# Performance work log

Hardware: AMD Instinct MI355X
Metric: run time of the kernel (lower is better)

The kernel has to match this reference:

```python
import jax, jax.numpy as jnp
import numpy as np

TOPK = 32

def topk_signed(x, k):
    # keep k entries with largest |value|, zero the rest (exactly k, scatter semantics)
    _, idx = jax.lax.top_k(jnp.abs(x), k)                       # [B, k]
    B = x.shape[0]
    mask = jnp.zeros(x.shape, dtype=bool).at[jnp.arange(B)[:, None], idx].set(True)
    return x * mask

def setup_inputs() -> dict:
    key = jax.random.key(0)
    k1, k2, k3 = jax.random.split(key, 3)
    B, D, L = 16384, 768, 16384
    x = jax.random.normal(k1, (B, D), dtype=jnp.float32)
    W_enc = jax.random.normal(k2, (L, D), dtype=jnp.float32) / np.sqrt(D)
    W_dec = jax.random.normal(k3, (D, L), dtype=jnp.float32) / np.sqrt(L)
    return {"x": x, "W_enc": W_enc, "W_dec": W_dec}

def reference(x, W_enc, W_dec):
    h = x @ W_enc.T                 # [B, L] encode (no bias)
    a = topk_signed(h, TOPK)        # [B, L] sparse latents
    recon = a @ W_dec.T             # [B, D] decode (no bias)
    return recon, a
```

## Files before the change

kernel.cpp:

```cpp
#include <hip/hip_runtime.h>


#define NB 16384
#define ND 768
#define NL 16384
#define SLOTS 24
#define NSL (64 * SLOTS)
#define ROWS 4
#define EPT 6
#define DLT 0.024f
#define CINB 0x40000000u
#define BNDB 0x20000000u
#define IMSK 0xffffu

typedef unsigned short u16;
typedef short bf16x8_t __attribute__((ext_vector_type(8)));
typedef float f32x4_t __attribute__((ext_vector_type(4)));
typedef unsigned short u16x4_t __attribute__((ext_vector_type(4)));

__device__ __forceinline__ u16 f2bf(float f) {
  union { float f; unsigned u; } x; x.f = f;
  unsigned r = x.u + 0x7fffu + ((x.u >> 16) & 1u);
  return (u16)(r >> 16);
}
__device__ __forceinline__ float bf2f(u16 u) {
  union { unsigned u; float f; } x; x.u = ((unsigned)u) << 16;
  return x.f;
}

__device__ __forceinline__ void async16(u16* lds, const u16* g) {
  __builtin_amdgcn_global_load_lds(
      (const __attribute__((address_space(1))) unsigned int*)g,
      (__attribute__((address_space(3))) unsigned int*)lds, 16, 0, 0);
}

__global__ __launch_bounds__(256) void cvt2_bf16(const float* __restrict__ s0,
                                                 u16* __restrict__ d0,
                                                 const float* __restrict__ s1,
                                                 u16* __restrict__ d1, int n4) {
  int i = blockIdx.x * 256 + threadIdx.x;
  const float* s; u16* d;
  if (i < n4) { s = s0; d = d0; } else { s = s1; d = d1; i -= n4; }
  const float4 v = ((const float4*)s)[i];
  u16x4_t o;
  o.x = f2bf(v.x); o.y = f2bf(v.y); o.z = f2bf(v.z); o.w = f2bf(v.w);
  ((u16x4_t*)d)[i] = o;
}

__global__ __launch_bounds__(512, 2) void enc_gemm(const u16* __restrict__ A,
                                                   const u16* __restrict__ Bm,
                                                   unsigned* __restrict__ Lst) {
  __shared__ u16 Ax[2][2][8192];
  __shared__ u16 Bx[2][2][8192];
  __shared__ unsigned rcnt[256];
  __shared__ unsigned slots[256 * SLOTS];

  const int tid  = threadIdx.x;
  const int lane = tid & 63;
  const int w    = tid >> 6;
  const int wr   = w >> 2;
  const int wc   = w & 3;

  const int linear = blockIdx.y * gridDim.x + blockIdx.x;
  const int xcd = linear & 7;
  const int j   = linear >> 3;
  const int hh  = j >> 8;
  const int jj  = j & 255;
  const int cg  = jj >> 5;
  const int rr_ = jj & 3;
  const int cc_ = (jj >> 2) & 7;
  const int brow = (xcd * 8 + hh * 4 + rr_) * 256;
  const int bcol = (cg * 8 + cc_) * 256;

  if (tid < 256) rcnt[tid] = 0;
#pragma unroll
  for (int i = 0; i < (256 * SLOTS) / 512; ++i) slots[tid + 512 * i] = 0;

  f32x4_t acc[8][4];
#pragma unroll
  for (int m = 0; m < 8; ++m)
#pragma unroll
    for (int n = 0; n < 4; ++n) acc[m][n] = (f32x4_t){0.f, 0.f, 0.f, 0.f};

  const int swz = ((lane & 7) ^ (lane >> 3)) * 8;
  const u16* gA = A  + (size_t)(brow + w * 16 + (lane >> 3)) * ND + swz;
  const u16* gB = Bm + (size_t)(bcol + w * 16 + (lane >> 3)) * ND + swz;

#define STGA(BUF, H, J, KT) \
  async16(&Ax[BUF][H][w * 1024 + (J) * 512], gA + ((H) * 128 + (J) * 8) * ND + (KT) * 64)
#define STGB(BUF, H, J, KT) \
  async16(&Bx[BUF][H][w * 1024 + (J) * 512], gB + ((H) * 128 + (J) * 8) * ND + (KT) * 64)
#define STG8(BUF, KT) { STGA(BUF,0,0,KT); STGA(BUF,0,1,KT); STGA(BUF,1,0,KT); STGA(BUF,1,1,KT); \
                        STGB(BUF,0,0,KT); STGB(BUF,0,1,KT); STGB(BUF,1,0,KT); STGB(BUF,1,1,KT); }

  const int fr  = lane & 15;
  const int q4  = lane >> 4;
  const int frl = fr & 7;
  const int c0  = ((q4)     ^ frl) * 8;
  const int c1  = ((4 + q4) ^ frl) * 8;
  const int bhalf = wc >> 1;
  const int brow0 = (wc & 1) * 64;

  STG8(0, 0);

  bf16x8_t afr[4][2];
  bf16x8_t bfr[2][2][2];

#define MFMA16(QR, QC)                                                        \
  __builtin_amdgcn_s_setprio(1);                                              \
  _Pragma("unroll")                                                           \
  for (int m2 = 0; m2 < 4; ++m2)                                              \
    _Pragma("unroll")                                                         \
    for (int n2 = 0; n2 < 2; ++n2) {                                          \
      acc[(QR)*4+m2][(QC)*2+n2] = __builtin_amdgcn_mfma_f32_16x16x32_bf16(    \
          afr[m2][0], bfr[QC][n2][0], acc[(QR)*4+m2][(QC)*2+n2], 0, 0, 0);    \
      acc[(QR)*4+m2][(QC)*2+n2] = __builtin_amdgcn_mfma_f32_16x16x32_bf16(    \
          afr[m2][1], bfr[QC][n2][1], acc[(QR)*4+m2][(QC)*2+n2], 0, 0, 0);    \
    }                                                                         \
  __builtin_amdgcn_s_setprio(0);

#define LDA(BUF, QR)                                                          \
  _Pragma("unroll")                                                           \
  for (int m2 = 0; m2 < 4; ++m2) {                                            \
    afr[m2][0] = *(const bf16x8_t*)&Ax[BUF][wr][((QR)*64 + m2*16 + fr)*64 + c0]; \
    afr[m2][1] = *(const bf16x8_t*)&Ax[BUF][wr][((QR)*64 + m2*16 + fr)*64 + c1]; \
  }
#define LDB(BUF, QC)                                                          \
  _Pragma("unroll")                                                           \
  for (int n2 = 0; n2 < 2; ++n2) {                                            \
    bfr[QC][n2][0] = *(const bf16x8_t*)&Bx[BUF][bhalf][(brow0 + (QC)*32 + n2*16 + fr)*64 + c0]; \
    bfr[QC][n2][1] = *(const bf16x8_t*)&Bx[BUF][bhalf][(brow0 + (QC)*32 + n2*16 + fr)*64 + c1]; \
  }

#define HALF(BUF)                                                              \
  __builtin_amdgcn_s_barrier();                   \
  __builtin_amdgcn_sched_barrier(0);                                           \
  LDA(BUF, 0); LDB(BUF, 0); MFMA16(0, 0);                                      \
  LDB(BUF, 1); MFMA16(0, 1);                                                   \
  LDA(BUF, 1); MFMA16(1, 0); MFMA16(1, 1);                                     \
  __builtin_amdgcn_s_barrier();

  for (int i = 0; i < 6; ++i) {
    const int kodd = 2 * i + 1, knxt = 2 * i + 2;
    STG8(1, kodd);
    asm volatile("s_waitcnt vmcnt(8)" ::: "memory");
    HALF(0);
    if (knxt < 12) {
      STG8(0, knxt);
      asm volatile("s_waitcnt vmcnt(8)" ::: "memory");
    } else {
      asm volatile("s_waitcnt vmcnt(0)" ::: "memory");
    }
    HALF(1);
  }
#undef HALF
#undef LDA
#undef LDB
#undef MFMA16
#undef STG8
#undef STGA
#undef STGB

  __syncthreads();

  const int r4 = (lane >> 4) * 4;
#pragma unroll
  for (int m = 0; m < 8; ++m)
#pragma unroll
    for (int n = 0; n < 4; ++n)
#pragma unroll
      for (int i = 0; i < 4; ++i) {
        const u16 hb = f2bf(acc[m][n][i]);
        if (fabsf(bf2f(hb)) >= 2.5f) {
          const int rl = wr * 128 + m * 16 + r4 + i;
          unsigned s = atomicAdd(&rcnt[rl], 1u);
          if (s < SLOTS)
            slots[rl * SLOTS + s] =
                ((unsigned)(bcol + wc * 64 + n * 16 + fr) << 16) | (unsigned)hb;
        }
      }
  __syncthreads();

  const int rl = tid >> 1, hf = tid & 1;
  unsigned* dst = Lst + (size_t)(brow + rl) * NL + 8192 + (bcol >> 8) * SLOTS + hf * 12;
  const unsigned* src = &slots[rl * SLOTS + hf * 12];
  ((uint4*)dst)[0] = ((const uint4*)src)[0];
  ((uint4*)dst)[1] = ((const uint4*)src)[1];
  ((uint4*)dst)[2] = ((const uint4*)src)[2];
}

__global__ __launch_bounds__(256) void transpose_wdec(const float* __restrict__ Wd,
                                                      u16* __restrict__ WdT) {
  __shared__ float tile[32][33];
  const int l0 = blockIdx.x * 32, d0 = blockIdx.y * 32;
  const int tx = threadIdx.x, ty = threadIdx.y;
#pragma unroll
  for (int i = 0; i < 4; ++i)
    tile[ty + 8 * i][tx] = Wd[(size_t)(d0 + ty + 8 * i) * NL + l0 + tx];
  __syncthreads();
#pragma unroll
  for (int i = 0; i < 4; ++i)
    WdT[(size_t)(l0 + ty + 8 * i) * ND + d0 + tx] = f2bf(tile[tx][ty + 8 * i]);
}

__global__ __launch_bounds__(256) void topk_decode(const unsigned* __restrict__ Lst,
                                                   const float* __restrict__ x,
                                                   const float* __restrict__ Wenc,
                                                   const u16* __restrict__ WdTb,
                                                   float* __restrict__ Aout,
                                                   float* __restrict__ recon) {
  const int r0 = blockIdx.x * ROWS;
  const int t  = threadIdx.x;
  __shared__ unsigned hist[ROWS][64];
  __shared__ unsigned cnt[ROWS];
  __shared__ float tcs[ROWS];
  __shared__ float b32v[ROWS];
  __shared__ int    cidx[ROWS][256];
  __shared__ float  cval[ROWS][256];
  __shared__ float  cabs[ROWS][256];
  __shared__ float  xs[ROWS][768];
  __shared__ int    selI[ROWS][32];
  __shared__ float  selV[ROWS][32];

  if (t < 64) {
#pragma unroll
    for (int rr = 0; rr < ROWS; ++rr) hist[rr][t] = 0;
  }
  if (t < ROWS) cnt[t] = 0;
#pragma unroll
  for (int rr = 0; rr < ROWS; ++rr) {
    cidx[rr][t] = (int)IMSK;
    cval[rr][t] = 0.0f; cabs[rr][t] = -1.0f;
  }

  unsigned ev[ROWS][EPT];
#pragma unroll
  for (int rr = 0; rr < ROWS; ++rr) {
    const unsigned* lrow = Lst + (size_t)(r0 + rr) * NL + 8192;
#pragma unroll
    for (int i = 0; i < EPT; ++i)
      ev[rr][i] = lrow[t + 256 * i];
    const float* xrow = x + (size_t)(r0 + rr) * ND;
    xs[rr][t] = xrow[t]; xs[rr][t + 256] = xrow[t + 256]; xs[rr][t + 512] = xrow[t + 512];
  }
  __syncthreads();

  const f32x4_t z4 = (f32x4_t){0.f, 0.f, 0.f, 0.f};
#pragma unroll
  for (int rr = 0; rr < ROWS; ++rr) {
    f32x4_t* arow4 = (f32x4_t*)(Aout + (size_t)(r0 + rr) * NL);
#pragma unroll
    for (int i = 0; i < NL / 4 / 256; ++i)
      __builtin_nontemporal_store(z4, arow4 + t + 256 * i);
  }

#pragma unroll
  for (int rr = 0; rr < ROWS; ++rr)
#pragma unroll
    for (int i = 0; i < EPT; ++i) {
      const float f = fabsf(bf2f((u16)(ev[rr][i] & 0xffffu)));
      if (f >= 2.0f) {
        int b = (int)((f - 2.0f) * 32.0f);
        if (b > 63) b = 63;
        atomicAdd(&hist[rr][b], 1u);
      }
    }
  __syncthreads();

  if (t < ROWS) {
    unsigned cum = 0; int b32 = 20;
    for (int b = 63; b >= 0; --b) { cum += hist[t][b]; if (cum >= 32u) { b32 = b; break; } }
    int bb = b32 - 3; if (bb < 17) bb = 17;
    tcs[t] = 2.0f + (float)bb * 0.03125f;
  }
  __syncthreads();

#pragma unroll
  for (int rr = 0; rr < ROWS; ++rr) {
    const float tc = tcs[rr];
#pragma unroll
    for (int i = 0; i < EPT; ++i) {
      const unsigned e = ev[rr][i];
      const float sv = bf2f((u16)(e & 0xffffu));
      const float f = fabsf(sv);
      if (f >= tc) {
        unsigned q = atomicAdd(&cnt[rr], 1u);
        if (q < 256u) { cidx[rr][q] = (int)(e >> 16); cval[rr][q] = sv; cabs[rr][q] = f; }
      }
    }
  }
  __syncthreads();

  {
    const int rw = t >> 6, sl = t & 63;
    const int ncr = min((int)cnt[rw], 256);
#pragma unroll
    for (int k2 = 0; k2 < 4; ++k2) {
      const int s = sl + 64 * k2;
      const float myA = cabs[rw][s];
      const int   myI = cidx[rw][s];
      int rank = 0;
      for (int jq = 0; jq < ncr; ++jq) {
        const float ja = cabs[rw][jq];
        const int   ji = cidx[rw][jq];
        rank += (ja > myA || (ja == myA && ji < myI)) ? 1 : 0;
      }
      if (s < ncr && rank == 31) b32v[rw] = myA;
    }
  }
  __syncthreads();

  {
    const int rw = t >> 6, sl = t & 63;
    const float b32 = b32v[rw];
    const float up = b32 + 2.0f * DLT, dn = b32 - 2.0f * DLT;
    const int ncr = min((int)cnt[rw], 256);
    for (int k2 = 0; k2 < 4; ++k2) {
      const int s = sl + 64 * k2;
      if (s >= ncr) continue;
      const float f = cabs[rw][s];
      if (f >= up) {
        cidx[rw][s] |= (int)CINB;
      } else if (f > dn) {
        const int myI = cidx[rw][s];
        cidx[rw][s] = myI | (int)BNDB;
        const float* wrow = Wenc + (size_t)myI * ND;
        float acc = 0.0f;
#pragma unroll 8
        for (int k = 0; k < ND; k += 4) {
          const float4 wv = *(const float4*)(wrow + k);
          acc = fmaf(xs[rw][k],     wv.x, acc);
          acc = fmaf(xs[rw][k + 1], wv.y, acc);
          acc = fmaf(xs[rw][k + 2], wv.z, acc);
          acc = fmaf(xs[rw][k + 3], wv.w, acc);
        }
        cval[rw][s] = acc;
        cabs[rw][s] = fabsf(acc);
      }
    }
  }
  __syncthreads();

  {
    const int rw = t >> 6, sl = t & 63;
    const int ncr = min((int)cnt[rw], 256);
#pragma unroll
    for (int k2 = 0; k2 < 4; ++k2) {
      const int s = sl + 64 * k2;
      if (s >= ncr) continue;
      const unsigned ce = (unsigned)cidx[rw][s];
      const bool myCin  = (ce & CINB) != 0u;
      const bool myBand = (ce & BNDB) != 0u;
      if (!(myCin || myBand)) continue;
      const int   myI = (int)(ce & IMSK);
      const float myA = cabs[rw][s];
      int rcin = 0, rband = 0, cincnt = 0;
      for (int jq = 0; jq < ncr; ++jq) {
        const unsigned je = (unsigned)cidx[rw][jq];
        const float ja = cabs[rw][jq];
        const int   ji = (int)(je & IMSK);
        const bool  jc = (je & CINB) != 0u;
        const bool  jb = (je & BNDB) != 0u;
        cincnt += jc ? 1 : 0;
        const bool beats = (ja > myA || (ja == myA && ji < myI));
        if (myCin && jc && beats) ++rcin;
        if (myBand && jb && beats) ++rband;
      }
      if (myCin) {
        selI[rw][rcin] = myI; selV[rw][rcin] = cval[rw][s];
      } else if (rband < 32 - cincnt) {
        selI[rw][cincnt + rband] = myI; selV[rw][cincnt + rband] = cval[rw][s];
      }
    }
  }
  __syncthreads();

  if (t < 128) {
    const int rr = t >> 5, s = t & 31;
    Aout[(size_t)(r0 + rr) * NL + selI[rr][s]] = selV[rr][s];
  }

  {
    const int rw = t >> 6;
    const int il = t & 63;
    float* rrow = recon + (size_t)(r0 + rw) * ND;
#pragma unroll
    for (int p = 0; p < 2; ++p) {
      const int c = p == 0 ? il : 64 + il;
      if (c < 96) {
        const int c0 = c * 8;
        float a[8] = {0.f, 0.f, 0.f, 0.f, 0.f, 0.f, 0.f, 0.f};
#pragma unroll 8
        for (int jq = 0; jq < 32; ++jq) {
          const bf16x8_t wv = *(const bf16x8_t*)(WdTb + (size_t)selI[rw][jq] * ND + c0);
          const float v = selV[rw][jq];
#pragma unroll
          for (int k = 0; k < 8; ++k) a[k] = fmaf(v, bf2f((u16)wv[k]), a[k]);
        }
        *(float4*)(rrow + c0)     = make_float4(a[0], a[1], a[2], a[3]);
        *(float4*)(rrow + c0 + 4) = make_float4(a[4], a[5], a[6], a[7]);
      }
    }
  }
}

extern "C" void kernel_launch(void* const* d_in, const int* in_sizes, int n_in,
                              void* d_out, int out_size, void* d_ws, size_t ws_size,
                              hipStream_t stream) {
  const float* x    = (const float*)d_in[0];
  const float* Wenc = (const float*)d_in[1];
  const float* Wdec = (const float*)d_in[2];

  float* out   = (float*)d_out;
  float* recon = out;
  float* abase = out + (size_t)NB * ND;

  const size_t szXB = (size_t)NB * ND * 2;
  const size_t szWB = (size_t)NL * ND * 2;
  const size_t szWT = (size_t)NL * ND * 2;
  const size_t need = szXB + szWB + szWT;
  if (ws_size < need) return;

  char* ws   = (char*)d_ws;
  u16*  xbf  = (u16*)ws;
  u16*  wbf  = (u16*)(ws + szXB);
  u16*  wdTb = (u16*)(ws + szXB + szWB);

  const int n4 = NB * ND / 4;
  cvt2_bf16<<<(2 * n4 + 255) / 256, 256, 0, stream>>>(x, xbf, Wenc, wbf, n4);
  enc_gemm<<<dim3(NL / 256, NB / 256), 512, 0, stream>>>(xbf, wbf, (unsigned*)abase);
  transpose_wdec<<<dim3(NL / 32, ND / 32), dim3(32, 8), 0, stream>>>(Wdec, wdTb);
  topk_decode<<<NB / ROWS, 256, 0, stream>>>((const unsigned*)abase, x, Wenc, wdTb, abase, recon);
}
```

Measured before the change: 951.7 us.

## Load encoder B fragments directly from global into registers, bypassing LDS

Drops the shared-memory staging buffer for the W_enc tile. Each wave now reads its B MFMA fragments straight from global memory into registers, one k-step ahead, while A is still staged through LDS with async copies. This saves half of the LDS footprint and the LDS reads and writes for B. In exchange, waves that share a column tile load the same B data twice, and the per-lane global loads are strided by row, so less global load latency may be hidden behind the MFMAs.

```diff
diff --git a/kernel.cpp b/kernel.cpp
--- a/kernel.cpp
+++ b/kernel.cpp
@@ -51,7 +51,6 @@
                                                    const u16* __restrict__ Bm,
                                                    unsigned* __restrict__ Lst) {
   __shared__ u16 Ax[2][2][8192];
-  __shared__ u16 Bx[2][2][8192];
   __shared__ unsigned rcnt[256];
   __shared__ unsigned slots[256 * SLOTS];
 
@@ -83,28 +82,31 @@
     for (int n = 0; n < 4; ++n) acc[m][n] = (f32x4_t){0.f, 0.f, 0.f, 0.f};
 
   const int swz = ((lane & 7) ^ (lane >> 3)) * 8;
-  const u16* gA = A  + (size_t)(brow + w * 16 + (lane >> 3)) * ND + swz;
-  const u16* gB = Bm + (size_t)(bcol + w * 16 + (lane >> 3)) * ND + swz;
+  const u16* gA = A + (size_t)(brow + w * 16 + (lane >> 3)) * ND + swz;
 
 #define STGA(BUF, H, J, KT) \
   async16(&Ax[BUF][H][w * 1024 + (J) * 512], gA + ((H) * 128 + (J) * 8) * ND + (KT) * 64)
-#define STGB(BUF, H, J, KT) \
-  async16(&Bx[BUF][H][w * 1024 + (J) * 512], gB + ((H) * 128 + (J) * 8) * ND + (KT) * 64)
-#define STG8(BUF, KT) { STGA(BUF,0,0,KT); STGA(BUF,0,1,KT); STGA(BUF,1,0,KT); STGA(BUF,1,1,KT); \
-                        STGB(BUF,0,0,KT); STGB(BUF,0,1,KT); STGB(BUF,1,0,KT); STGB(BUF,1,1,KT); }
+#define STG4A(BUF, KT) { STGA(BUF,0,0,KT); STGA(BUF,0,1,KT); STGA(BUF,1,0,KT); STGA(BUF,1,1,KT); }
 
   const int fr  = lane & 15;
   const int q4  = lane >> 4;
   const int frl = fr & 7;
   const int c0  = ((q4)     ^ frl) * 8;
   const int c1  = ((4 + q4) ^ frl) * 8;
-  const int bhalf = wc >> 1;
-  const int brow0 = (wc & 1) * 64;
-
-  STG8(0, 0);
+
+  const u16* pB = Bm + (size_t)(bcol + wc * 64 + fr) * ND + q4 * 8;
 
   bf16x8_t afr[4][2];
   bf16x8_t bfr[2][2][2];
+
+#define BL(KT)                                                                \
+  _Pragma("unroll")                                                           \
+  for (int qc = 0; qc < 2; ++qc)                                              \
+    _Pragma("unroll")                                                         \
+    for (int n2 = 0; n2 < 2; ++n2)                                            \
+      _Pragma("unroll")                                                       \
+      for (int ks = 0; ks < 2; ++ks)                                          \
+        bfr[qc][n2][ks] = *(const bf16x8_t*)(pB + (size_t)(qc * 32 + n2 * 16) * ND + (KT) * 64 + ks * 32);
 
 #define MFMA16(QR, QC)                                                        \
   __builtin_amdgcn_s_setprio(1);                                              \
@@ -125,41 +127,38 @@
     afr[m2][0] = *(const bf16x8_t*)&Ax[BUF][wr][((QR)*64 + m2*16 + fr)*64 + c0]; \
     afr[m2][1] = *(const bf16x8_t*)&Ax[BUF][wr][((QR)*64 + m2*16 + fr)*64 + c1]; \
   }
-#define LDB(BUF, QC)                                                          \
-  _Pragma("unroll")                                                           \
-  for (int n2 = 0; n2 < 2; ++n2) {                                            \
-    bfr[QC][n2][0] = *(const bf16x8_t*)&Bx[BUF][bhalf][(brow0 + (QC)*32 + n2*16 + fr)*64 + c0]; \
-    bfr[QC][n2][1] = *(const bf16x8_t*)&Bx[BUF][bhalf][(brow0 + (QC)*32 + n2*16 + fr)*64 + c1]; \
-  }
-
-#define HALF(BUF)                                                              \
-  __builtin_amdgcn_s_barrier();                   \
-  __builtin_amdgcn_sched_barrier(0);                                           \
-  LDA(BUF, 0); LDB(BUF, 0); MFMA16(0, 0);                                      \
-  LDB(BUF, 1); MFMA16(0, 1);                                                   \
-  LDA(BUF, 1); MFMA16(1, 0); MFMA16(1, 1);                                     \
-  __builtin_amdgcn_s_barrier();
+
+  STG4A(0, 0);
+  BL(0);
 
   for (int i = 0; i < 6; ++i) {
     const int kodd = 2 * i + 1, knxt = 2 * i + 2;
-    STG8(1, kodd);
-    asm volatile("s_waitcnt vmcnt(8)" ::: "memory");
-    HALF(0);
+    STG4A(1, kodd);
+    asm volatile("s_waitcnt vmcnt(4)" ::: "memory");
+    __builtin_amdgcn_s_barrier();
+    __builtin_amdgcn_sched_barrier(0);
+    LDA(0, 0); MFMA16(0, 0); MFMA16(0, 1);
+    LDA(0, 1); MFMA16(1, 0); MFMA16(1, 1);
+    BL(kodd);
+    __builtin_amdgcn_s_barrier();
     if (knxt < 12) {
-      STG8(0, knxt);
-      asm volatile("s_waitcnt vmcnt(8)" ::: "memory");
+      STG4A(0, knxt);
+      asm volatile("s_waitcnt vmcnt(4)" ::: "memory");
     } else {
       asm volatile("s_waitcnt vmcnt(0)" ::: "memory");
     }
-    HALF(1);
-  }
-#undef HALF
+    __builtin_amdgcn_s_barrier();
+    __builtin_amdgcn_sched_barrier(0);
+    LDA(1, 0); MFMA16(0, 0); MFMA16(0, 1);
+    LDA(1, 1); MFMA16(1, 0); MFMA16(1, 1);
+    if (knxt < 12) BL(knxt);
+    __builtin_amdgcn_s_barrier();
+  }
 #undef LDA
-#undef LDB
 #undef MFMA16
-#undef STG8
+#undef BL
+#undef STG4A
 #undef STGA
-#undef STGB
 
   __syncthreads();
 
```

Measured after the change: 1.148 ms. 20.6% more time.
